# Kernel tuning notes

Measured on AMD Instinct MI355X. Metric: run time of the kernel, lower is better.

## Reference

```python
import jax, jax.numpy as jnp
import numpy as np
from jax import lax

N, M, K = 192, 192, 3
B, H, W = 16, 16, 16
MK = M * K


def _deconv(x, w, b):
    # PyTorch ConvTranspose2d(k=5, stride=2, padding=2, output_padding=1)
    # == dilated conv with flipped kernel, pads (k-1-p, k-1-p+op) = (2, 3)
    wt = jnp.flip(w, (2, 3)).transpose(1, 0, 2, 3)  # (in,out,kh,kw) -> (out,in,kh,kw)
    y = lax.conv_general_dilated(x, wt, (1, 1), [(2, 3), (2, 3)],
                                 lhs_dilation=(2, 2),
                                 dimension_numbers=('NCHW', 'OIHW', 'NCHW'))
    return y + b[None, :, None, None]


def _conv(x, w, b, pad):
    y = lax.conv_general_dilated(x, w, (1, 1), [(pad, pad), (pad, pad)],
                                 dimension_numbers=('NCHW', 'OIHW', 'NCHW'))
    return y + b[None, :, None, None]


def _leaky(x):
    return jnp.where(x >= 0, x, 0.01 * x)


def setup_inputs() -> dict:
    key = jax.random.key(0)
    ks = jax.random.split(key, 19)
    s = 0.02
    d = {
        'z1': jax.random.normal(ks[0], (B, N, H, W), jnp.float32),
        # gmm_sigma branch
        'gs_w1': jax.random.normal(ks[1], (N, N, 5, 5), jnp.float32) * s,
        'gs_b1': jnp.zeros((N,), jnp.float32),
        'gs_w2': jax.random.normal(ks[2], (N, N, 5, 5), jnp.float32) * s,
        'gs_b2': jnp.zeros((N,), jnp.float32),
        'gs_w3': jax.random.normal(ks[3], (MK, N, 5, 5), jnp.float32) * s,
        'gs_b3': jnp.zeros((MK,), jnp.float32),
        # gmm_means branch
        'gm_w1': jax.random.normal(ks[4], (N, N, 5, 5), jnp.float32) * s,
        'gm_b1': jnp.zeros((N,), jnp.float32),
        'gm_w2': jax.random.normal(ks[5], (N, N, 5, 5), jnp.float32) * s,
        'gm_b2': jnp.zeros((N,), jnp.float32),
        'gm_w3': jax.random.normal(ks[6], (MK, N, 5, 5), jnp.float32) * s,
        'gm_b3': jnp.zeros((MK,), jnp.float32),
        # gmm_weights branch
        'gw_w1': jax.random.normal(ks[7], (N, N, 5, 5), jnp.float32) * s,
        'gw_b1': jnp.zeros((N,), jnp.float32),
        'gw_w2': jax.random.normal(ks[8], (N, MK, 5, 5), jnp.float32) * s,
        'gw_b2': jnp.zeros((MK,), jnp.float32),
        'gw_w3': jax.random.normal(ks[9], (MK, MK, 1, 1), jnp.float32) * s,
        'gw_b3': jnp.zeros((MK,), jnp.float32),
    }
    return d


def reference(z1, gs_w1, gs_b1, gs_w2, gs_b2, gs_w3, gs_b3,
              gm_w1, gm_b1, gm_w2, gm_b2, gm_w3, gm_b3,
              gw_w1, gw_b1, gw_w2, gw_b2, gw_w3, gw_b3):
    # sigma: deconv, ReLU, deconv, ReLU, conv(k5,s1), ReLU
    s = jax.nn.relu(_deconv(z1, gs_w1, gs_b1))
    s = jax.nn.relu(_deconv(s, gs_w2, gs_b2))
    sigma = jax.nn.relu(_conv(s, gs_w3, gs_b3, 2))
    # means: deconv, LeakyReLU, deconv, LeakyReLU, conv(k5,s1)
    m = _leaky(_deconv(z1, gm_w1, gm_b1))
    m = _leaky(_deconv(m, gm_w2, gm_b2))
    means = _conv(m, gm_w3, gm_b3, 2)
    # weights: deconv, LeakyReLU, deconv, global-max-pool, LeakyReLU, conv1x1
    w = _leaky(_deconv(z1, gw_w1, gw_b1))
    w = _deconv(w, gw_w2, gw_b2)
    w = jnp.max(w, axis=(2, 3), keepdims=True)  # fused replacement of the B*C python loop
    w = _leaky(w)
    w = _conv(w, gw_w3, gw_b3, 0)  # (B, M*K, 1, 1)
    temp = w.reshape(-1, K, M, 1, 1)
    temp = jax.nn.softmax(temp, axis=1)  # softmax over the K mixture components
    weights = temp.reshape(-1, MK, 1, 1)
    return (sigma, means, weights)
```

## Files before the change

kernel.cpp:

```cpp
#include <hip/hip_runtime.h>
#include <hip/hip_bf16.h>
#include <math.h>

typedef __attribute__((ext_vector_type(8))) short bf16x8;
typedef __attribute__((ext_vector_type(4))) float f32x4;
typedef __attribute__((ext_vector_type(16))) float f32x16;
typedef __attribute__((ext_vector_type(4))) unsigned short ushort4v;

constexpr int Bsz = 16;

__device__ __forceinline__ float act_r(float v, int a) {
  if (a == 1) return v > 0.f ? v : 0.f;
  if (a == 2) return v >= 0.f ? v : 0.01f * v;
  return v;
}

__device__ __forceinline__ unsigned short f2bf(float x) {
  __hip_bfloat16 h = __float2bfloat16(x);
  return __builtin_bit_cast(unsigned short, h);
}

__device__ __forceinline__ void gll16(const unsigned short* g, unsigned short* l) {
  __builtin_amdgcn_global_load_lds(
      (const __attribute__((address_space(1))) unsigned int*)g,
      (__attribute__((address_space(3))) unsigned int*)l, 16, 0, 0);
}

__global__ __launch_bounds__(256) void zprep_k(
    const float* __restrict__ z, unsigned short* __restrict__ zh)
{
  const int g = blockIdx.x * 256 + threadIdx.x;
  if (g >= 16 * 192 * 256) return;
  const int b  = g / 49152;
  const int rr = g - b * 49152;
  const int px = rr / 192;
  const int ic = rr - px * 192;
  const int o = ((b * 6 + (ic >> 5)) * 256 + px) * 32 + (ic & 31);
  zh[o] = f2bf(z[(b * 192 + ic) * 256 + px]);
}

__device__ __forceinline__ void dprep_one(
    const float* __restrict__ w, unsigned short* __restrict__ wh, int OC, int g)
{
  const int oc  = g % OC;
  const int rem = g / OC;
  const int icb = rem % 24;
  const int j   = rem / 24;
  bf16x8 hv;
  #pragma unroll
  for (int e = 0; e < 8; ++e)
    hv[e] = (short)f2bf(w[((icb * 8 + e) * OC + oc) * 25 + j]);
  *(bf16x8*)&wh[((j * 24 + icb) * OC + oc) * 8] = hv;
}

__global__ __launch_bounds__(256) void wprep1_k(
    const float* __restrict__ s0, const float* __restrict__ s1,
    const float* __restrict__ s2, unsigned short* __restrict__ wh)
{
  const int bid = blockIdx.x;
  const int seg = bid / 450;
  const int g   = (bid - seg * 450) * 256 + threadIdx.x;
  if (g >= 192 * 24 * 25) return;
  const float* src = seg == 0 ? s0 : (seg == 1 ? s1 : s2);
  dprep_one(src, wh + (size_t)seg * 921600, 192, g);
}

__global__ __launch_bounds__(256) void wprep_d_k(
    const float* __restrict__ w, unsigned short* __restrict__ wh, int OC)
{
  const int g = blockIdx.x * 256 + threadIdx.x;
  if (g >= OC * 24 * 25) return;
  dprep_one(w, wh, OC, g);
}

__global__ __launch_bounds__(256) void wprep_t_k(
    const float* __restrict__ w, unsigned short* __restrict__ wh)
{
  const int g = blockIdx.x * 256 + threadIdx.x;
  if (g >= 576 * 24 * 25) return;
  const int oc  = g % 576;
  const int rem = g / 576;
  const int icb = rem % 24;
  const int j   = rem / 24;
  bf16x8 hv;
  #pragma unroll
  for (int e = 0; e < 8; ++e)
    hv[e] = (short)f2bf(w[oc * 4800 + (icb * 8 + e) * 25 + j]);
  *(bf16x8*)&wh[((j * 24 + icb) * 576 + oc) * 8] = hv;
}

template<int H, int OMODE, int OL>
__global__ __launch_bounds__(256, 2) void deconv2_k(
    const unsigned short* __restrict__ xh, long x_brs,
    const unsigned short* __restrict__ wh, long w_brs,
    const float* __restrict__ b0, const float* __restrict__ b1,
    const float* __restrict__ b2,
    unsigned short* __restrict__ yh, long y_brs,
    float* __restrict__ mvp, int OC, int a0, int a1, int a2)
{
  constexpr int NF = H / 16;
  __shared__ __align__(16) unsigned short xs[10][H + 2][32];
  __shared__ float red[4][32];

  const int zz = blockIdx.z;
  const int br = zz >> 4;
  const int b  = zz & 15;
  const int by = blockIdx.y;
  const int r0 = by * 8;
  const int oc0 = blockIdx.x * 32;
  const int t  = threadIdx.x;
  const int wv = t >> 6;
  const int l  = t & 63;
  const int lg = l >> 4;
  const int ln = l & 15;

  const unsigned short* xhp = xh + (long)br * x_brs;
  const unsigned short* whp = wh + (long)br * w_brs;
  const float* bias = br == 0 ? b0 : (br == 1 ? b1 : b2);
  const int act = br == 0 ? a0 : (br == 1 ? a1 : a2);

  f32x4 acc[2][4][2][NF];
  #pragma unroll
  for (int rr = 0; rr < 2; ++rr)
    #pragma unroll
    for (int p = 0; p < 4; ++p)
      #pragma unroll
      for (int of = 0; of < 2; ++of)
        #pragma unroll
        for (int nf = 0; nf < NF; ++nf)
          acc[rr][p][of][nf] = (f32x4){0.f, 0.f, 0.f, 0.f};

  const bf16x8 zero8 = {0,0,0,0,0,0,0,0};

  for (int c = 0; c < 6; ++c) {
    __syncthreads();
    constexpr int DC = 10 * H * 4;
    #pragma unroll
    for (int k = 0; k < (DC + 255) / 256; ++k) {
      const int li = t + k * 256;
      if (li < DC) {
        const int part = li & 3;
        const int col  = (li >> 2) & (H - 1);
        const int row  = li / (4 * H);
        const int y    = r0 - 1 + row;
        bf16x8 v = zero8;
        if ((unsigned)y < (unsigned)H)
          v = *(const bf16x8*)&xhp[(((size_t)(b * 6 + c) * H + y) * H + col) * 32 + part * 8];
        *(bf16x8*)&xs[row][col + 1][part * 8] = v;
      }
    }
    if (t < 80) {
      const int row = t >> 3;
      const int cc  = t & 7;
      const int col = (cc >> 2) ? (H + 1) : 0;
      *(bf16x8*)&xs[row][col][(cc & 3) * 8] = zero8;
    }
    __syncthreads();

    #pragma unroll
    for (int j = 0; j < 25; ++j) {
      const int ky = j / 5, kx = j % 5;
      const int sy = ky & 1, sx = kx & 1;
      const int dy = (2 + sy - ky) / 2;
      const int dx = (2 + sx - kx) / 2;
      const int p  = sy * 2 + sx;

      bf16x8 ah[2];
      const int wbase = ((j * 24 + c * 4 + lg) * OC + oc0 + ln) * 8;
      #pragma unroll
      for (int of = 0; of < 2; ++of)
        ah[of] = *(const bf16x8*)&whp[wbase + of * 128];
      #pragma unroll
      for (int rr = 0; rr < 2; ++rr) {
        const int rl = 2 * wv + rr + 1 + dy;
        bf16x8 bh[NF];
        #pragma unroll
        for (int nf = 0; nf < NF; ++nf) {
          const int cl = 1 + nf * 16 + ln + dx;
          bh[nf] = *(const bf16x8*)&xs[rl][cl][lg * 8];
        }
        #pragma unroll
        for (int of = 0; of < 2; ++of)
          #pragma unroll
          for (int nf = 0; nf < NF; ++nf)
            acc[rr][p][of][nf] = __builtin_amdgcn_mfma_f32_16x16x32_bf16(
                ah[of], bh[nf], acc[rr][p][of][nf], 0, 0, 0);
      }
    }
  }

  if (OMODE == 1) {
    const int OCG = OC >> 5;
    float bv[2][4];
    #pragma unroll
    for (int of = 0; of < 2; ++of)
      #pragma unroll
      for (int r = 0; r < 4; ++r)
        bv[of][r] = bias[oc0 + of * 16 + lg * 4 + r];
    unsigned short* yhp = yh + (long)br * y_brs;
    #pragma unroll
    for (int rr = 0; rr < 2; ++rr) {
      const int iy = r0 + 2 * wv + rr;
      #pragma unroll
      for (int sy = 0; sy < 2; ++sy)
        #pragma unroll
        for (int sx = 0; sx < 2; ++sx) {
          const int p  = sy * 2 + sx;
          const int oy = 2 * iy + sy;
          #pragma unroll
          for (int of = 0; of < 2; ++of) {
            const int ocb = oc0 + of * 16 + lg * 4;
            const int cg  = ocb >> 5;
            const int co  = ocb & 31;
            #pragma unroll
            for (int nf = 0; nf < NF; ++nf) {
              const int ox = 2 * (nf * 16 + ln) + sx;
              ushort4v hv;
              #pragma unroll
              for (int r = 0; r < 4; ++r)
                hv[r] = f2bf(act_r(acc[rr][p][of][nf][r] + bv[of][r], act));
              size_t idx;
              if (OL) {
                const int qg = cg * 4 + (co >> 3);
                idx = (((size_t)(b * (OC >> 3) + qg) * (4 * H * H)) +
                       (size_t)oy * (2 * H) + ox) * 8 + (co & 7);
              } else {
                idx = (((size_t)(b * OCG + cg) * (4 * H * H)) +
                       (size_t)oy * (2 * H) + ox) * 32 + co;
              }
              *(ushort4v*)&yhp[idx] = hv;
            }
          }
        }
    }
  } else {
    #pragma unroll
    for (int of = 0; of < 2; ++of)
      #pragma unroll
      for (int r = 0; r < 4; ++r) {
        float m = -3.402823466e38f;
        #pragma unroll
        for (int rr = 0; rr < 2; ++rr)
          #pragma unroll
          for (int p = 0; p < 4; ++p)
            #pragma unroll
            for (int nf = 0; nf < NF; ++nf)
              m = fmaxf(m, acc[rr][p][of][nf][r]);
        #pragma unroll
        for (int off = 1; off < 16; off <<= 1)
          m = fmaxf(m, __shfl_xor(m, off));
        if (ln == 0)
          red[wv][of * 16 + lg * 4 + r] = m + bias[oc0 + of * 16 + lg * 4 + r];
      }
    __syncthreads();
    if (t < 32) {
      const float v = fmaxf(fmaxf(red[0][t], red[1][t]), fmaxf(red[2][t], red[3][t]));
      mvp[((b * 4) + by) * OC + oc0 + t] = v;
    }
  }
}

__global__ __launch_bounds__(256, 3) void conv3_k(
    const unsigned short* __restrict__ gxh,
    const unsigned short* __restrict__ gwh,
    const float* __restrict__ bias, float* __restrict__ out, int act)
{
  __shared__ __align__(16) unsigned short xs[8][4][68][8];

  const int bid  = blockIdx.x;
  const int orig = (bid & 7) * 288 + (bid >> 3);
  const int ocg  = orig >> 8;
  const int rem  = orig & 255;
  const int b    = rem >> 4;
  const int band = rem & 15;
  const int y0   = band * 4;
  const int oc0  = ocg * 64;
  const int t    = threadIdx.x;
  const int wv   = t >> 6;
  const int l    = t & 63;
  const int lg   = l >> 4;
  const int ln   = l & 15;

  f32x4 acc[4][4];
  #pragma unroll
  for (int of = 0; of < 4; ++of)
    #pragma unroll
    for (int pf = 0; pf < 4; ++pf)
      acc[of][pf] = (f32x4){0.f, 0.f, 0.f, 0.f};

  {
    unsigned short* fx = (unsigned short*)xs;
    const bf16x8 z8 = {0,0,0,0,0,0,0,0};
    #pragma unroll
    for (int k = 0; k < 9; ++k) {
      const int li = t + k * 256;
      if (li < 2176) *(bf16x8*)&fx[li * 8] = z8;
    }
  }

  for (int c = 0; c < 6; ++c) {
    __syncthreads();
    #pragma unroll
    for (int k = 0; k < 8; ++k) {
      const int idx = k * 4 + wv;
      const int row = idx >> 2, q = idx & 3;
      const int y = y0 - 2 + row;
      if ((unsigned)y < 64u) {
        const unsigned short* g = &gxh[
            ((((size_t)b * 24 + c * 4 + q) << 12) + ((size_t)y << 6) + l) * 8];
        gll16(g, &xs[row][q][2][0]);
      }
    }
    __syncthreads();

    #pragma unroll
    for (int j = 0; j < 25; ++j) {
      const int ky = j / 5, kx = j % 5;
      bf16x8 ah[4], bx[4];
      const int wbase = ((j * 24 + c * 4 + lg) * 576 + oc0 + ln) * 8;
      #pragma unroll
      for (int of = 0; of < 4; ++of)
        ah[of] = *(const bf16x8*)&gwh[wbase + of * 128];
      const int rl = wv + ky;
      #pragma unroll
      for (int pf = 0; pf < 4; ++pf)
        bx[pf] = *(const bf16x8*)&xs[rl][lg][pf * 16 + ln + kx][0];
      #pragma unroll
      for (int of = 0; of < 4; ++of)
        #pragma unroll
        for (int pf = 0; pf < 4; ++pf)
          acc[of][pf] = __builtin_amdgcn_mfma_f32_16x16x32_bf16(
              ah[of], bx[pf], acc[of][pf], 0, 0, 0);
    }
  }

  const int y = y0 + wv;
  #pragma unroll
  for (int of = 0; of < 4; ++of)
    #pragma unroll
    for (int r = 0; r < 4; ++r) {
      const int oc = oc0 + of * 16 + lg * 4 + r;
      const float bv = bias[oc];
      float* po = &out[(((size_t)(b * 576 + oc) * 64) + y) * 64 + ln];
      #pragma unroll
      for (int pf = 0; pf < 4; ++pf)
        po[16 * pf] = act_r(acc[of][pf][r] + bv, act);
    }
}

__global__ __launch_bounds__(256) void head_k(
    const float* __restrict__ mvp, const float* __restrict__ w3,
    const float* __restrict__ b3, float* __restrict__ outw)
{
  __shared__ float lv[576];
  __shared__ float yv[576];
  const int b = blockIdx.x;
  const int t = threadIdx.x;
  for (int i = t; i < 576; i += 256) {
    float m = mvp[(b * 4 + 0) * 576 + i];
    #pragma unroll
    for (int ti = 1; ti < 4; ++ti)
      m = fmaxf(m, mvp[(b * 4 + ti) * 576 + i]);
    lv[i] = m >= 0.f ? m : 0.01f * m;
  }
  __syncthreads();
  for (int oc = t; oc < 576; oc += 256) {
    float s = b3[oc];
    for (int c = 0; c < 576; ++c) s += w3[oc * 576 + c] * lv[c];
    yv[oc] = s;
  }
  __syncthreads();
  if (t < 192) {
    const float v0 = yv[t], v1 = yv[192 + t], v2 = yv[384 + t];
    const float mx = fmaxf(v0, fmaxf(v1, v2));
    const float e0 = expf(v0 - mx), e1 = expf(v1 - mx), e2 = expf(v2 - mx);
    const float inv = 1.f / (e0 + e1 + e2);
    outw[b * 576 + t]       = e0 * inv;
    outw[b * 576 + 192 + t] = e1 * inv;
    outw[b * 576 + 384 + t] = e2 * inv;
  }
}

extern "C" void kernel_launch(void* const* d_in, const int* in_sizes, int n_in,
                              void* d_out, int out_size, void* d_ws, size_t ws_size,
                              hipStream_t stream)
{
  (void)in_sizes; (void)n_in; (void)out_size; (void)ws_size;

  const float* z1    = (const float*)d_in[0];
  const float* gs_w1 = (const float*)d_in[1];
  const float* gs_b1 = (const float*)d_in[2];
  const float* gs_w2 = (const float*)d_in[3];
  const float* gs_b2 = (const float*)d_in[4];
  const float* gs_w3 = (const float*)d_in[5];
  const float* gs_b3 = (const float*)d_in[6];
  const float* gm_w1 = (const float*)d_in[7];
  const float* gm_b1 = (const float*)d_in[8];
  const float* gm_w2 = (const float*)d_in[9];
  const float* gm_b2 = (const float*)d_in[10];
  const float* gm_w3 = (const float*)d_in[11];
  const float* gm_b3 = (const float*)d_in[12];
  const float* gw_w1 = (const float*)d_in[13];
  const float* gw_b1 = (const float*)d_in[14];
  const float* gw_w2 = (const float*)d_in[15];
  const float* gw_b2 = (const float*)d_in[16];
  const float* gw_w3 = (const float*)d_in[17];
  const float* gw_b3 = (const float*)d_in[18];

  unsigned short* p = (unsigned short*)d_ws;
  unsigned short* Z   = p; p += 786432;
  unsigned short* A1  = p; p += (size_t)3 * 3145728;
  unsigned short* A2  = p; p += 12582912;
  unsigned short* W1  = p; p += (size_t)3 * 921600;
  unsigned short* Wb  = p; p += 2764800;
  float* MVp = (float*)p;

  float* o_sigma = (float*)d_out;
  float* o_means = o_sigma + (size_t)Bsz * 576 * 64 * 64;
  float* o_w     = o_means + (size_t)Bsz * 576 * 64 * 64;

  dim3 blk(256);

  zprep_k<<<dim3(3072), blk, 0, stream>>>(z1, Z);
  wprep1_k<<<dim3(1350), blk, 0, stream>>>(gs_w1, gm_w1, gw_w1, W1);

  deconv2_k<16,1,0><<<dim3(6,2,48), blk, 0, stream>>>(
      Z, 0, W1, 921600, gs_b1, gm_b1, gw_b1,
      A1, 3145728, nullptr, 192, 1, 2, 2);

  wprep_d_k<<<dim3(450), blk, 0, stream>>>(gs_w2, Wb, 192);
  deconv2_k<32,1,1><<<dim3(6,4,16), blk, 0, stream>>>(
      A1, 0, Wb, 0, gs_b2, gs_b2, gs_b2,
      A2, 0, nullptr, 192, 1, 1, 1);
  wprep_t_k<<<dim3(1350), blk, 0, stream>>>(gs_w3, Wb);
  conv3_k<<<dim3(2304), blk, 0, stream>>>(A2, Wb, gs_b3, o_sigma, 1);

  wprep_d_k<<<dim3(450), blk, 0, stream>>>(gm_w2, Wb, 192);
  deconv2_k<32,1,1><<<dim3(6,4,16), blk, 0, stream>>>(
      A1 + (size_t)3145728, 0, Wb, 0, gm_b2, gm_b2, gm_b2,
      A2, 0, nullptr, 192, 2, 2, 2);
  wprep_t_k<<<dim3(1350), blk, 0, stream>>>(gm_w3, Wb);
  conv3_k<<<dim3(2304), blk, 0, stream>>>(A2, Wb, gm_b3, o_means, 0);

  wprep_d_k<<<dim3(1350), blk, 0, stream>>>(gw_w2, Wb, 576);
  deconv2_k<32,2,0><<<dim3(18,4,16), blk, 0, stream>>>(
      A1 + (size_t)2 * 3145728, 0, Wb, 0,
      gw_b2, gw_b2, gw_b2, nullptr, 0, MVp, 576, 0, 0, 0);
  head_k<<<dim3(16), blk, 0, stream>>>(MVp, gw_w3, gw_b3, o_w);
}
```

Before: 1.161 ms.

## Double-buffer conv3 operand loads, stagger rows per wave, and retile deconv2 rows

In conv3_k, the weight and LDS operand loads for the next kernel tap are now issued before the MFMAs of the current tap, using two register buffers. MFMA issue priority is raised while those MFMAs run. Each wave's ky order is rotated by its wave index, and the LDS row stride is padded from 68 to 80, both to spread bank and cache access. The deconv2 kernel gains a rows-per-wave template parameter, and the sigma and means second-layer deconvs drop to one row per wave with twice the grid rows, trading fewer accumulators for more blocks and higher halo overhead.

After: 1.044 ms. 10.0% less time.

```diff
diff --git a/kernel.cpp b/kernel.cpp
--- a/kernel.cpp
+++ b/kernel.cpp
@@ -89,7 +89,7 @@
   *(bf16x8*)&wh[((j * 24 + icb) * 576 + oc) * 8] = hv;
 }
 
-template<int H, int OMODE, int OL>
+template<int H, int OMODE, int OL, int RPW>
 __global__ __launch_bounds__(256, 2) void deconv2_k(
     const unsigned short* __restrict__ xh, long x_brs,
     const unsigned short* __restrict__ wh, long w_brs,
@@ -99,14 +99,15 @@
     float* __restrict__ mvp, int OC, int a0, int a1, int a2)
 {
   constexpr int NF = H / 16;
-  __shared__ __align__(16) unsigned short xs[10][H + 2][32];
+  constexpr int R  = 4 * RPW;
+  __shared__ __align__(16) unsigned short xs[R + 2][H + 2][32];
   __shared__ float red[4][32];
 
   const int zz = blockIdx.z;
   const int br = zz >> 4;
   const int b  = zz & 15;
   const int by = blockIdx.y;
-  const int r0 = by * 8;
+  const int r0 = by * R;
   const int oc0 = blockIdx.x * 32;
   const int t  = threadIdx.x;
   const int wv = t >> 6;
@@ -119,9 +120,9 @@
   const float* bias = br == 0 ? b0 : (br == 1 ? b1 : b2);
   const int act = br == 0 ? a0 : (br == 1 ? a1 : a2);
 
-  f32x4 acc[2][4][2][NF];
-  #pragma unroll
-  for (int rr = 0; rr < 2; ++rr)
+  f32x4 acc[RPW][4][2][NF];
+  #pragma unroll
+  for (int rr = 0; rr < RPW; ++rr)
     #pragma unroll
     for (int p = 0; p < 4; ++p)
       #pragma unroll
@@ -134,7 +135,7 @@
 
   for (int c = 0; c < 6; ++c) {
     __syncthreads();
-    constexpr int DC = 10 * H * 4;
+    constexpr int DC = (R + 2) * H * 4;
     #pragma unroll
     for (int k = 0; k < (DC + 255) / 256; ++k) {
       const int li = t + k * 256;
@@ -149,7 +150,7 @@
         *(bf16x8*)&xs[row][col + 1][part * 8] = v;
       }
     }
-    if (t < 80) {
+    if (t < 8 * (R + 2)) {
       const int row = t >> 3;
       const int cc  = t & 7;
       const int col = (cc >> 2) ? (H + 1) : 0;
@@ -171,8 +172,8 @@
       for (int of = 0; of < 2; ++of)
         ah[of] = *(const bf16x8*)&whp[wbase + of * 128];
       #pragma unroll
-      for (int rr = 0; rr < 2; ++rr) {
-        const int rl = 2 * wv + rr + 1 + dy;
+      for (int rr = 0; rr < RPW; ++rr) {
+        const int rl = RPW * wv + rr + 1 + dy;
         bf16x8 bh[NF];
         #pragma unroll
         for (int nf = 0; nf < NF; ++nf) {
@@ -199,8 +200,8 @@
         bv[of][r] = bias[oc0 + of * 16 + lg * 4 + r];
     unsigned short* yhp = yh + (long)br * y_brs;
     #pragma unroll
-    for (int rr = 0; rr < 2; ++rr) {
-      const int iy = r0 + 2 * wv + rr;
+    for (int rr = 0; rr < RPW; ++rr) {
+      const int iy = r0 + RPW * wv + rr;
       #pragma unroll
       for (int sy = 0; sy < 2; ++sy)
         #pragma unroll
@@ -240,7 +241,7 @@
       for (int r = 0; r < 4; ++r) {
         float m = -3.402823466e38f;
         #pragma unroll
-        for (int rr = 0; rr < 2; ++rr)
+        for (int rr = 0; rr < RPW; ++rr)
           #pragma unroll
           for (int p = 0; p < 4; ++p)
             #pragma unroll
@@ -265,7 +266,7 @@
     const unsigned short* __restrict__ gwh,
     const float* __restrict__ bias, float* __restrict__ out, int act)
 {
-  __shared__ __align__(16) unsigned short xs[8][4][68][8];
+  __shared__ __align__(16) unsigned short xs[8][4][80][8];
 
   const int bid  = blockIdx.x;
   const int orig = (bid & 7) * 288 + (bid >> 3);
@@ -288,13 +289,20 @@
     for (int pf = 0; pf < 4; ++pf)
       acc[of][pf] = (f32x4){0.f, 0.f, 0.f, 0.f};
 
+  int ky2v[5], rlv[5];
+  #pragma unroll
+  for (int ky = 0; ky < 5; ++ky) {
+    int k2 = ky + wv; if (k2 >= 5) k2 -= 5;
+    ky2v[ky] = k2; rlv[ky] = wv + k2;
+  }
+
   {
     unsigned short* fx = (unsigned short*)xs;
     const bf16x8 z8 = {0,0,0,0,0,0,0,0};
     #pragma unroll
-    for (int k = 0; k < 9; ++k) {
+    for (int k = 0; k < 10; ++k) {
       const int li = t + k * 256;
-      if (li < 2176) *(bf16x8*)&fx[li * 8] = z8;
+      if (li < 2560) *(bf16x8*)&fx[li * 8] = z8;
     }
   }
 
@@ -313,25 +321,46 @@
     }
     __syncthreads();
 
+    const unsigned short* wrow = gwh + ((size_t)((c * 4 + lg) * 576) + oc0 + ln) * 8;
+    const unsigned short* xrow[5];
+    #pragma unroll
+    for (int ky = 0; ky < 5; ++ky)
+      xrow[ky] = &xs[rlv[ky]][lg][ln][0];
+
+    bf16x8 ah[2][4], bx[2][4];
+
+    #define LDW(KY, KX, S)                                                  \
+      {                                                                     \
+        const unsigned short* wj = wrow + (size_t)(ky2v[KY] * 5 + (KX)) * 110592; \
+        _Pragma("unroll")                                                   \
+        for (int of = 0; of < 4; ++of)                                      \
+          ah[S][of] = *(const bf16x8*)&wj[of * 128];                        \
+        const unsigned short* xr = xrow[KY];                                \
+        _Pragma("unroll")                                                   \
+        for (int pf = 0; pf < 4; ++pf)                                      \
+          bx[S][pf] = *(const bf16x8*)&xr[(pf * 16 + (KX)) * 8];            \
+      }
+
+    LDW(0, 0, 0)
     #pragma unroll
     for (int j = 0; j < 25; ++j) {
-      const int ky = j / 5, kx = j % 5;
-      bf16x8 ah[4], bx[4];
-      const int wbase = ((j * 24 + c * 4 + lg) * 576 + oc0 + ln) * 8;
-      #pragma unroll
-      for (int of = 0; of < 4; ++of)
-        ah[of] = *(const bf16x8*)&gwh[wbase + of * 128];
-      const int rl = wv + ky;
-      #pragma unroll
-      for (int pf = 0; pf < 4; ++pf)
-        bx[pf] = *(const bf16x8*)&xs[rl][lg][pf * 16 + ln + kx][0];
+      const int s = j & 1;
+      if (j < 24) {
+        const int jn = j + 1;
+        const int kyn = jn / 5, kxn = jn % 5;
+        const int ns = jn & 1;
+        LDW(kyn, kxn, ns)
+      }
+      __builtin_amdgcn_s_setprio(1);
       #pragma unroll
       for (int of = 0; of < 4; ++of)
         #pragma unroll
         for (int pf = 0; pf < 4; ++pf)
           acc[of][pf] = __builtin_amdgcn_mfma_f32_16x16x32_bf16(
-              ah[of], bx[pf], acc[of][pf], 0, 0, 0);
-    }
+              ah[s][of], bx[s][pf], acc[of][pf], 0, 0, 0);
+      __builtin_amdgcn_s_setprio(0);
+    }
+    #undef LDW
   }
 
   const int y = y0 + wv;
@@ -424,26 +453,26 @@
   zprep_k<<<dim3(3072), blk, 0, stream>>>(z1, Z);
   wprep1_k<<<dim3(1350), blk, 0, stream>>>(gs_w1, gm_w1, gw_w1, W1);
 
-  deconv2_k<16,1,0><<<dim3(6,2,48), blk, 0, stream>>>(
+  deconv2_k<16,1,0,2><<<dim3(6,2,48), blk, 0, stream>>>(
       Z, 0, W1, 921600, gs_b1, gm_b1, gw_b1,
       A1, 3145728, nullptr, 192, 1, 2, 2);
 
   wprep_d_k<<<dim3(450), blk, 0, stream>>>(gs_w2, Wb, 192);
-  deconv2_k<32,1,1><<<dim3(6,4,16), blk, 0, stream>>>(
+  deconv2_k<32,1,1,1><<<dim3(6,8,16), blk, 0, stream>>>(
       A1, 0, Wb, 0, gs_b2, gs_b2, gs_b2,
       A2, 0, nullptr, 192, 1, 1, 1);
   wprep_t_k<<<dim3(1350), blk, 0, stream>>>(gs_w3, Wb);
   conv3_k<<<dim3(2304), blk, 0, stream>>>(A2, Wb, gs_b3, o_sigma, 1);
 
   wprep_d_k<<<dim3(450), blk, 0, stream>>>(gm_w2, Wb, 192);
-  deconv2_k<32,1,1><<<dim3(6,4,16), blk, 0, stream>>>(
+  deconv2_k<32,1,1,1><<<dim3(6,8,16), blk, 0, stream>>>(
       A1 + (size_t)3145728, 0, Wb, 0, gm_b2, gm_b2, gm_b2,
       A2, 0, nullptr, 192, 2, 2, 2);
   wprep_t_k<<<dim3(1350), blk, 0, stream>>>(gm_w3, Wb);
   conv3_k<<<dim3(2304), blk, 0, stream>>>(A2, Wb, gm_b3, o_means, 0);
 
   wprep_d_k<<<dim3(1350), blk, 0, stream>>>(gw_w2, Wb, 576);
-  deconv2_k<32,2,0><<<dim3(18,4,16), blk, 0, stream>>>(
+  deconv2_k<32,2,0,2><<<dim3(18,4,16), blk, 0, stream>>>(
       A1 + (size_t)2 * 3145728, 0, Wb, 0,
       gw_b2, gw_b2, gw_b2, nullptr, 0, MVp, 576, 0, 0, 0);
   head_k<<<dim3(16), blk, 0, stream>>>(MVp, gw_w3, gw_b3, o_w);
```
